# Kernel tuning notes

Measured on AMD Instinct MI355X. Metric: run time of the kernel, lower is better.

The kernel has to match this reference:

```python
import jax, jax.numpy as jnp
import numpy as np
import math

VOCAB = 32000
DIM = 1024
TOKENS = 4096
PAD_IDX = 0
NBITS = 4
QN = -(2 ** (NBITS - 1))        # -8
QP = 2 ** (NBITS - 1) - 1       # 7


def setup_inputs() -> dict:
    key = jax.random.key(0)
    k_idx, k_w = jax.random.split(key)
    idx = jax.random.randint(k_idx, (TOKENS,), 0, VOCAB)
    # x is one-hot over the vocabulary, as implied by topk(x,1)[1] extracting the index
    x = jax.nn.one_hot(idx, VOCAB, dtype=jnp.float32)
    weight = jax.random.normal(k_w, (DIM, VOCAB), dtype=jnp.float32) * 0.02
    # LSQ init rule: alpha = 2 * mean|W| / sqrt(Qp)
    alpha = (2.0 * jnp.mean(jnp.abs(weight)) / math.sqrt(QP)).reshape(1)
    return {"x": x, "weight": weight, "alpha": alpha}


def reference(x, weight, alpha):
    # topk(x, 1)[1] on a one-hot input == argmax over vocab
    idx = jnp.argmax(x, axis=-1)                       # [T]
    mask = (idx == PAD_IDX)[:, None]                   # [T, 1]
    a = alpha[0]
    # LSQ fake-quantize the weight: round(clamp(w/alpha, Qn, Qp)) * alpha
    w_q = jnp.round(jnp.clip(weight / a, QN, QP)) * a  # [DIM, VOCAB]
    out = jnp.einsum('tv,dv->td', x, w_q)              # [T, DIM]
    return jnp.where(mask, 0.0, out)
```

## Files before the change

### kernel.cpp

```cpp
#include <hip/hip_runtime.h>


typedef float v4f __attribute__((ext_vector_type(4)));

constexpr int VOCAB  = 32000;
constexpr int DIM    = 1024;
constexpr int TOKENS = 4096;
constexpr int V4     = VOCAB / 4;
constexpr int WAVE   = 64;
constexpr int FULL_ITERS = V4 / 256;
constexpr int TAIL_BASE  = FULL_ITERS * 256;

__device__ __forceinline__ int check4(v4f v, int chunk) {
    if (v.x > 0.5f) return 4 * chunk + 0;
    if (v.y > 0.5f) return 4 * chunk + 1;
    if (v.z > 0.5f) return 4 * chunk + 2;
    if (v.w > 0.5f) return 4 * chunk + 3;
    return -1;
}

__global__ __launch_bounds__(WAVE) void emb_lsq_kernel(
    const float* __restrict__ x,
    const float* __restrict__ w,
    const float* __restrict__ alpha,
    float* __restrict__ out)
{
    const int t    = blockIdx.x;
    const int lane = threadIdx.x;

    const v4f* xr = reinterpret_cast<const v4f*>(x + (size_t)t * VOCAB);
    int found = -1;
    for (int k = 0; k < FULL_ITERS; ++k) {
        const int i = lane + 256 * k;
        v4f a0 = xr[i];
        v4f a1 = xr[i +  64];
        v4f a2 = xr[i + 128];
        v4f a3 = xr[i + 192];
        int f;
        if ((f = check4(a0, i      )) >= 0) found = f;
        else if ((f = check4(a1, i +  64)) >= 0) found = f;
        else if ((f = check4(a2, i + 128)) >= 0) found = f;
        else if ((f = check4(a3, i + 192)) >= 0) found = f;
        if (__ballot(found >= 0)) break;
    }
    if (!__ballot(found >= 0)) {
        v4f a = xr[TAIL_BASE + lane];
        found = check4(a, TAIL_BASE + lane);
    }
    unsigned long long m = __ballot(found >= 0);
    const int idx = m ? __shfl(found, (int)__ffsll(m) - 1) : -1;

    v4f* orow = reinterpret_cast<v4f*>(out + (size_t)t * DIM);
    if (idx <= 0) {
        v4f z = 0.f;
        #pragma unroll
        for (int j = 0; j < 4; ++j) orow[lane + 64 * j] = z;
    } else {
        const float a = alpha[0];
        const size_t col = (size_t)idx;
        float wv[16];
        #pragma unroll
        for (int j = 0; j < 4; ++j) {
            const int d0 = 4 * lane + 256 * j;
            wv[4*j+0] = w[(size_t)(d0 + 0) * VOCAB + col];
            wv[4*j+1] = w[(size_t)(d0 + 1) * VOCAB + col];
            wv[4*j+2] = w[(size_t)(d0 + 2) * VOCAB + col];
            wv[4*j+3] = w[(size_t)(d0 + 3) * VOCAB + col];
        }
        #pragma unroll
        for (int j = 0; j < 4; ++j) {
            v4f q;
            q.x = rintf(fminf(fmaxf(wv[4*j+0] / a, -8.f), 7.f)) * a;
            q.y = rintf(fminf(fmaxf(wv[4*j+1] / a, -8.f), 7.f)) * a;
            q.z = rintf(fminf(fmaxf(wv[4*j+2] / a, -8.f), 7.f)) * a;
            q.w = rintf(fminf(fmaxf(wv[4*j+3] / a, -8.f), 7.f)) * a;
            orow[lane + 64 * j] = q;
        }
    }
}

extern "C" void kernel_launch(void* const* d_in, const int* in_sizes, int n_in,
                              void* d_out, int out_size, void* d_ws, size_t ws_size,
                              hipStream_t stream) {
    const float* x     = (const float*)d_in[0];
    const float* w     = (const float*)d_in[1];
    const float* alpha = (const float*)d_in[2];
    float* out         = (float*)d_out;

    emb_lsq_kernel<<<TOKENS, WAVE, 0, stream>>>(x, w, alpha, out);
}
```

Measured before the change: 721.9 us.

## Split argmax scan into per-token vocab segments with early-exit done flags

Each token's vocabulary scan is split into 8 segments, each handled by its own wavefront, so the grid grows from 4096 to 32768 blocks. Each segment issues all of its x loads up front instead of walking the row serially with a ballot after every step. A per-token flag in workspace, zeroed by a memset, lets later segments skip their scan once an earlier block has found the hot index. This trades a serial per-token chain for more parallelism and memory-level concurrency, at the cost of an extra memset launch and atomics. Segments whose block is already in flight may still scan their full range.

```diff
diff --git a/kernel.cpp b/kernel.cpp
--- a/kernel.cpp
+++ b/kernel.cpp
@@ -3,79 +3,95 @@
 
 typedef float v4f __attribute__((ext_vector_type(4)));
 
-constexpr int VOCAB  = 32000;
-constexpr int DIM    = 1024;
-constexpr int TOKENS = 4096;
-constexpr int V4     = VOCAB / 4;
-constexpr int WAVE   = 64;
-constexpr int FULL_ITERS = V4 / 256;
-constexpr int TAIL_BASE  = FULL_ITERS * 256;
+constexpr int VOCAB   = 32000;
+constexpr int DIM     = 1024;
+constexpr int TOKENS  = 4096;
+constexpr int WAVE    = 64;
+constexpr int SEG_FLT = 4096;
+constexpr int NSEG    = (VOCAB + SEG_FLT - 1) / SEG_FLT;
+constexpr int FULL_ITERS = SEG_FLT / 4 / WAVE;
+constexpr int TAIL_FLT   = VOCAB - (NSEG - 1) * SEG_FLT;
+constexpr int TAIL_ITERS = TAIL_FLT / 4 / WAVE;
 
-__device__ __forceinline__ int check4(v4f v, int chunk) {
-    if (v.x > 0.5f) return 4 * chunk + 0;
-    if (v.y > 0.5f) return 4 * chunk + 1;
-    if (v.z > 0.5f) return 4 * chunk + 2;
-    if (v.w > 0.5f) return 4 * chunk + 3;
-    return -1;
-}
-
-__global__ __launch_bounds__(WAVE) void emb_lsq_kernel(
+__global__ __launch_bounds__(WAVE) void emb_lsq_seg(
     const float* __restrict__ x,
     const float* __restrict__ w,
     const float* __restrict__ alpha,
-    float* __restrict__ out)
+    float* __restrict__ out,
+    int* __restrict__ done)
 {
-    const int t    = blockIdx.x;
+    const int bid  = blockIdx.x;
+    const int seg  = bid >> 12;
+    const int t    = bid & (TOKENS - 1);
     const int lane = threadIdx.x;
 
-    const v4f* xr = reinterpret_cast<const v4f*>(x + (size_t)t * VOCAB);
+    if (seg > 0 &&
+        __hip_atomic_load(done + t, __ATOMIC_RELAXED, __HIP_MEMORY_SCOPE_AGENT) != 0)
+        return;
+
+    const int  base = seg * SEG_FLT;
+    const v4f* xr   = reinterpret_cast<const v4f*>(x + (size_t)t * VOCAB + base);
+
     int found = -1;
-    for (int k = 0; k < FULL_ITERS; ++k) {
-        const int i = lane + 256 * k;
-        v4f a0 = xr[i];
-        v4f a1 = xr[i +  64];
-        v4f a2 = xr[i + 128];
-        v4f a3 = xr[i + 192];
-        int f;
-        if ((f = check4(a0, i      )) >= 0) found = f;
-        else if ((f = check4(a1, i +  64)) >= 0) found = f;
-        else if ((f = check4(a2, i + 128)) >= 0) found = f;
-        else if ((f = check4(a3, i + 192)) >= 0) found = f;
-        if (__ballot(found >= 0)) break;
+    if (seg < NSEG - 1) {
+        v4f v[FULL_ITERS];
+        #pragma unroll
+        for (int j = 0; j < FULL_ITERS; ++j) v[j] = xr[lane + WAVE * j];
+        #pragma unroll
+        for (int j = 0; j < FULL_ITERS; ++j) {
+            const int p = base + 4 * (lane + WAVE * j);
+            if (v[j].x > 0.5f) found = p + 0;
+            if (v[j].y > 0.5f) found = p + 1;
+            if (v[j].z > 0.5f) found = p + 2;
+            if (v[j].w > 0.5f) found = p + 3;
+        }
+    } else {
+        v4f v[TAIL_ITERS];
+        #pragma unroll
+        for (int j = 0; j < TAIL_ITERS; ++j) v[j] = xr[lane + WAVE * j];
+        #pragma unroll
+        for (int j = 0; j < TAIL_ITERS; ++j) {
+            const int p = base + 4 * (lane + WAVE * j);
+            if (v[j].x > 0.5f) found = p + 0;
+            if (v[j].y > 0.5f) found = p + 1;
+            if (v[j].z > 0.5f) found = p + 2;
+            if (v[j].w > 0.5f) found = p + 3;
+        }
     }
-    if (!__ballot(found >= 0)) {
-        v4f a = xr[TAIL_BASE + lane];
-        found = check4(a, TAIL_BASE + lane);
-    }
-    unsigned long long m = __ballot(found >= 0);
-    const int idx = m ? __shfl(found, (int)__ffsll(m) - 1) : -1;
+
+    const unsigned long long m = __ballot(found >= 0);
+    if (!m) return;
+
+    if (lane == 0) atomicExch(done + t, 1);
+    const int idx = __shfl(found, (int)__ffsll((long long)m) - 1);
 
     v4f* orow = reinterpret_cast<v4f*>(out + (size_t)t * DIM);
-    if (idx <= 0) {
+    if (idx == 0) {
         v4f z = 0.f;
         #pragma unroll
-        for (int j = 0; j < 4; ++j) orow[lane + 64 * j] = z;
-    } else {
-        const float a = alpha[0];
-        const size_t col = (size_t)idx;
-        float wv[16];
-        #pragma unroll
-        for (int j = 0; j < 4; ++j) {
-            const int d0 = 4 * lane + 256 * j;
-            wv[4*j+0] = w[(size_t)(d0 + 0) * VOCAB + col];
-            wv[4*j+1] = w[(size_t)(d0 + 1) * VOCAB + col];
-            wv[4*j+2] = w[(size_t)(d0 + 2) * VOCAB + col];
-            wv[4*j+3] = w[(size_t)(d0 + 3) * VOCAB + col];
-        }
-        #pragma unroll
-        for (int j = 0; j < 4; ++j) {
-            v4f q;
-            q.x = rintf(fminf(fmaxf(wv[4*j+0] / a, -8.f), 7.f)) * a;
-            q.y = rintf(fminf(fmaxf(wv[4*j+1] / a, -8.f), 7.f)) * a;
-            q.z = rintf(fminf(fmaxf(wv[4*j+2] / a, -8.f), 7.f)) * a;
-            q.w = rintf(fminf(fmaxf(wv[4*j+3] / a, -8.f), 7.f)) * a;
-            orow[lane + 64 * j] = q;
-        }
+        for (int j = 0; j < 4; ++j) orow[lane + WAVE * j] = z;
+        return;
+    }
+
+    const float  a   = alpha[0];
+    const size_t col = (size_t)idx;
+    float wv[16];
+    #pragma unroll
+    for (int j = 0; j < 4; ++j) {
+        const int d0 = 4 * lane + 256 * j;
+        wv[4*j+0] = w[(size_t)(d0 + 0) * VOCAB + col];
+        wv[4*j+1] = w[(size_t)(d0 + 1) * VOCAB + col];
+        wv[4*j+2] = w[(size_t)(d0 + 2) * VOCAB + col];
+        wv[4*j+3] = w[(size_t)(d0 + 3) * VOCAB + col];
+    }
+    #pragma unroll
+    for (int j = 0; j < 4; ++j) {
+        v4f q;
+        q.x = rintf(fminf(fmaxf(wv[4*j+0] / a, -8.f), 7.f)) * a;
+        q.y = rintf(fminf(fmaxf(wv[4*j+1] / a, -8.f), 7.f)) * a;
+        q.z = rintf(fminf(fmaxf(wv[4*j+2] / a, -8.f), 7.f)) * a;
+        q.w = rintf(fminf(fmaxf(wv[4*j+3] / a, -8.f), 7.f)) * a;
+        orow[lane + WAVE * j] = q;
     }
 }
 
@@ -86,6 +102,8 @@
     const float* w     = (const float*)d_in[1];
     const float* alpha = (const float*)d_in[2];
     float* out         = (float*)d_out;
+    int*   done        = (int*)d_ws;
 
-    emb_lsq_kernel<<<TOKENS, WAVE, 0, stream>>>(x, w, alpha, out);
+    hipMemsetAsync(done, 0, TOKENS * sizeof(int), stream);
+    emb_lsq_seg<<<TOKENS * NSEG, WAVE, 0, stream>>>(x, w, alpha, out, done);
 }
```

Result: no change. 734.9 us (+1.8%).
